# Optimization experiments

Measured on AMD Instinct MI355X. Metric: run time of the kernel, lower is better.

The kernel has to match this reference:

```python
import jax, jax.numpy as jnp
import numpy as np
from jax import lax

D = 1024      # embedding_dim
E = 8         # num_experts
F = 4096      # expert_dim
TOP_K = 2


def setup_inputs() -> dict:
    key = jax.random.key(0)
    ks = jax.random.split(key, 8)
    s = 0.02
    return {
        "x": jax.random.normal(ks[0], (4, 2048, D), dtype=jnp.float32),
        "gate_w": jax.random.normal(ks[1], (D, E), dtype=jnp.float32) * s,
        "gate_b": jnp.zeros((E,), dtype=jnp.float32),
        "w1": jax.random.normal(ks[2], (E, D, F), dtype=jnp.float32) * s,
        "b1": jnp.zeros((E, F), dtype=jnp.float32),
        "w2": jax.random.normal(ks[3], (E, F, D), dtype=jnp.float32) * s,
        "b2": jnp.zeros((E, D), dtype=jnp.float32),
    }


def reference(x, gate_w, gate_b, w1, b1, w2, b2):
    B, S, _ = x.shape
    flat = x.reshape(-1, D)                      # [T, D]
    T = flat.shape[0]

    # Router: top-k gating with softmax over the selected logits (in fp32)
    logits = flat @ gate_w + gate_b              # [T, E]
    topv, topi = lax.top_k(logits, TOP_K)        # [T, K]
    topw = jax.nn.softmax(topv.astype(jnp.float32), axis=-1).astype(x.dtype)
    routing = jnp.zeros_like(logits).at[jnp.arange(T)[:, None], topi].set(topw)  # [T, E]

    # Per-expert MLP, combined with routing weights (zeros for unselected experts
    # reproduce the masked gather/scatter of the original exactly).
    def body(acc, params):
        W1e, b1e, W2e, b2e, we = params          # we: [T]
        h = jax.nn.gelu(flat @ W1e + b1e, approximate=False)  # [T, F]
        out = h @ W2e + b2e                      # [T, D]
        return acc + out * we[:, None], None

    init = jnp.zeros_like(flat)
    final, _ = lax.scan(body, init, (w1, b1, w2, b2, routing.T))
    return final.reshape(B, S, D)
```

## Files before the change

### kernel.cpp

```cpp
#include <hip/hip_runtime.h>
#include <hip/hip_bf16.h>
#include <math.h>


#define TK 8192
#define DDIM 1024
#define FDIM 4096
#define NEXP 8
#define MAXT128 136

typedef unsigned short u16;
typedef __attribute__((ext_vector_type(8))) short bf16x8;
typedef __attribute__((ext_vector_type(4))) float f32x4;

typedef const __attribute__((address_space(1))) unsigned int* gp_u32;
typedef __attribute__((address_space(3))) unsigned int* lp_u32;

__device__ __forceinline__ u16 f2bf(float f) {
  unsigned x = __float_as_uint(f);
  x += 0x7fffu + ((x >> 16) & 1u);
  return (u16)(x >> 16);
}

__device__ __forceinline__ float fast_gelu(float v) {
  float p = v * (1.5957691216f + 0.0713548162f * v * v);
  float t = __expf(p);
  return v * t * __builtin_amdgcn_rcpf(t + 1.0f);
}

__device__ __forceinline__ bf16x8 ldfrag(const char* base, int row, int slot) {
  return *(const bf16x8*)(base + row * 128 + ((slot ^ (row & 7)) << 4));
}

__global__ void router_kernel(const float* __restrict__ x, const float* __restrict__ gw,
                              const float* __restrict__ gb,
                              int* __restrict__ top_e, float* __restrict__ top_w) {
  const int t = blockIdx.x;
  const int l = threadIdx.x;
  const float* xr = x + (size_t)t * DDIM;
  float acc[8] = {0, 0, 0, 0, 0, 0, 0, 0};
  for (int k = l; k < DDIM; k += 64) {
    float xv = xr[k];
    const float4* g4 = (const float4*)(gw + (size_t)k * 8);
    float4 ga = g4[0], gbv = g4[1];
    acc[0] = fmaf(xv, ga.x, acc[0]);  acc[1] = fmaf(xv, ga.y, acc[1]);
    acc[2] = fmaf(xv, ga.z, acc[2]);  acc[3] = fmaf(xv, ga.w, acc[3]);
    acc[4] = fmaf(xv, gbv.x, acc[4]); acc[5] = fmaf(xv, gbv.y, acc[5]);
    acc[6] = fmaf(xv, gbv.z, acc[6]); acc[7] = fmaf(xv, gbv.w, acc[7]);
  }
#pragma unroll
  for (int e = 0; e < 8; ++e)
#pragma unroll
    for (int m = 32; m; m >>= 1) acc[e] += __shfl_xor(acc[e], m, 64);
  if (l == 0) {
    float lg[8];
#pragma unroll
    for (int e = 0; e < 8; ++e) lg[e] = acc[e] + gb[e];
    int i1 = 0;
#pragma unroll
    for (int e = 1; e < 8; ++e) if (lg[e] > lg[i1]) i1 = e;
    int i2 = (i1 == 0) ? 1 : 0;
#pragma unroll
    for (int e = 0; e < 8; ++e) if (e != i1 && lg[e] > lg[i2]) i2 = e;
    float e2 = __expf(lg[i2] - lg[i1]);
    float inv = 1.0f / (1.0f + e2);
    top_e[2 * t] = i1;      top_e[2 * t + 1] = i2;
    top_w[2 * t] = inv;     top_w[2 * t + 1] = e2 * inv;
  }
}

__global__ void count_kernel(const int* __restrict__ top_e, int* __restrict__ counts) {
  __shared__ int lc[8];
  if (threadIdx.x < 8) lc[threadIdx.x] = 0;
  __syncthreads();
  int t = blockIdx.x * 256 + threadIdx.x;
  if (t < TK) {
    atomicAdd(&lc[top_e[2 * t]], 1);
    atomicAdd(&lc[top_e[2 * t + 1]], 1);
  }
  __syncthreads();
  if (threadIdx.x < 8) atomicAdd(&counts[threadIdx.x], lc[threadIdx.x]);
}

__global__ void scan_kernel(const int* __restrict__ counts, int* __restrict__ seg,
                            int* __restrict__ cur, int* __restrict__ nt128,
                            int* __restrict__ map128) {
  if (threadIdx.x == 0) {
    int s = 0, i128 = 0;
    for (int e = 0; e < 8; ++e) {
      seg[e] = s; cur[e] = s;
      int c = counts[e];
      for (int mt = 0; mt * 128 < c; ++mt) map128[i128++] = (e << 16) | mt;
      s += c;
    }
    seg[8] = s;
    *nt128 = i128;
  }
}

__global__ void scatter_kernel(const int* __restrict__ top_e, const float* __restrict__ top_w,
                               int* __restrict__ cur, int* __restrict__ tok_ids,
                               float* __restrict__ tok_wt, int* __restrict__ inv) {
  __shared__ int lcnt[8];
  __shared__ int lbase[8];
  if (threadIdx.x < 8) lcnt[threadIdx.x] = 0;
  __syncthreads();
  int t = blockIdx.x * 256 + threadIdx.x;
  int e[2]; float wv[2]; int lpos[2];
  bool valid = t < TK;
  if (valid) {
#pragma unroll
    for (int j = 0; j < 2; ++j) {
      e[j] = top_e[2 * t + j];
      wv[j] = top_w[2 * t + j];
      lpos[j] = atomicAdd(&lcnt[e[j]], 1);
    }
  }
  __syncthreads();
  if (threadIdx.x < 8) lbase[threadIdx.x] = atomicAdd(&cur[threadIdx.x], lcnt[threadIdx.x]);
  __syncthreads();
  if (valid) {
#pragma unroll
    for (int j = 0; j < 2; ++j) {
      int slot = lbase[e[j]] + lpos[j];
      tok_ids[slot] = t;
      tok_wt[slot] = wv[j];
      inv[2 * t + j] = slot;
    }
  }
}

__global__ void gather_cast_kernel(const float* __restrict__ x, const int* __restrict__ tok_ids,
                                   uint4* __restrict__ Xg) {
  int idx = blockIdx.x * 256 + threadIdx.x;
  int row = idx >> 7, c8 = (idx & 127) * 8;
  long tok = tok_ids[row];
  const float4* p = (const float4*)(x + tok * DDIM + c8);
  float4 a = p[0], b = p[1];
  uint4 o;
  o.x = (unsigned)f2bf(a.x) | ((unsigned)f2bf(a.y) << 16);
  o.y = (unsigned)f2bf(a.z) | ((unsigned)f2bf(a.w) << 16);
  o.z = (unsigned)f2bf(b.x) | ((unsigned)f2bf(b.y) << 16);
  o.w = (unsigned)f2bf(b.z) | ((unsigned)f2bf(b.w) << 16);
  Xg[idx] = o;
}

__global__ void transpose_cast_kernel(const float* __restrict__ src, u16* __restrict__ dst,
                                      int K, int N) {
  __shared__ u16 tile[64][66];
  const int t = threadIdx.x;
  const float* s = src + (size_t)blockIdx.z * K * N + (size_t)(blockIdx.x * 64) * N + blockIdx.y * 64;
  u16* d = dst + (size_t)blockIdx.z * N * K + (size_t)(blockIdx.y * 64) * K + blockIdx.x * 64;
#pragma unroll
  for (int r = 0; r < 4; ++r) {
    int idx = r * 256 + t;
    int kk = idx >> 4, nn4 = (idx & 15) * 4;
    float4 v = *(const float4*)(s + (size_t)kk * N + nn4);
    tile[kk][nn4 + 0] = f2bf(v.x);
    tile[kk][nn4 + 1] = f2bf(v.y);
    tile[kk][nn4 + 2] = f2bf(v.z);
    tile[kk][nn4 + 3] = f2bf(v.w);
  }
  __syncthreads();
#pragma unroll
  for (int r = 0; r < 2; ++r) {
    int idx = r * 256 + t;
    int nn = idx >> 3, kk8 = (idx & 7) * 8;
    uint4 o;
    o.x = (unsigned)tile[kk8 + 0][nn] | ((unsigned)tile[kk8 + 1][nn] << 16);
    o.y = (unsigned)tile[kk8 + 2][nn] | ((unsigned)tile[kk8 + 3][nn] << 16);
    o.z = (unsigned)tile[kk8 + 4][nn] | ((unsigned)tile[kk8 + 5][nn] << 16);
    o.w = (unsigned)tile[kk8 + 6][nn] | ((unsigned)tile[kk8 + 7][nn] << 16);
    *(uint4*)(d + (size_t)nn * K + kk8) = o;
  }
}

template <int PHASE, int BM, int BN, int CHA, int CHB>
__global__ __launch_bounds__(256, 4) void moe_gemm(
    const u16* __restrict__ A, const u16* __restrict__ Bt,
    const float* __restrict__ bias, u16* __restrict__ Hout,
    u16* __restrict__ Yout,
    const int* __restrict__ seg_off, const int* __restrict__ counts,
    const int* __restrict__ ntiles, const int* __restrict__ tile_map,
    int K, int N) {
  constexpr int MF = BM / 32;
  constexpr int NF = BN / 32;

  const int NTm = *ntiles;
  const int nb = N / BN;
  const int nwg = NTm * nb;
  const int bid = (int)blockIdx.x;
  if (bid >= nwg) return;
  const int q = nwg >> 3, rr = nwg & 7;
  const int xcd = bid & 7, pos = bid >> 3;
  const int work = xcd * q + (xcd < rr ? xcd : rr) + pos;
  const int mtIdx = work / nb;
  const int n0 = (work % nb) * BN;

  const int ent = tile_map[mtIdx];
  const int e = ent >> 16;
  const int mt = ent & 0xffff;
  const int cnt = counts[e];
  const int seg = seg_off[e];

  const int t = threadIdx.x;
  const int w = t >> 6;
  const int l = t & 63;
  const int lr = l & 15, lh = l >> 4;
  const int wr = w >> 1, wc = w & 1;

  __shared__ u16 As[BM * 64];
  __shared__ u16 Bs[BN * 64];

  const u16* aga[CHA];
  const u16* bga[CHB];
  const u16* Bte = Bt + (size_t)e * N * K;
#pragma unroll
  for (int j = 0; j < CHA; ++j) {
    int c = t + 256 * j;
    int row = c >> 3;
    int js = (c & 7) ^ (row & 7);
    int m = mt * BM + row;
    if (m >= cnt) m = cnt - 1;
    aga[j] = A + (size_t)(seg + m) * K + js * 8;
  }
#pragma unroll
  for (int j = 0; j < CHB; ++j) {
    int c = t + 256 * j;
    int row = c >> 3;
    int js = (c & 7) ^ (row & 7);
    bga[j] = Bte + (size_t)(n0 + row) * K + js * 8;
  }

  f32x4 acc[MF][NF];
#pragma unroll
  for (int i = 0; i < MF; ++i)
#pragma unroll
    for (int j = 0; j < NF; ++j) acc[i][j] = (f32x4){0.f, 0.f, 0.f, 0.f};

  const int NT = K / 64;
  for (int kt = 0; kt < NT; ++kt) {
#pragma unroll
    for (int j = 0; j < CHA; ++j)
      __builtin_amdgcn_global_load_lds((gp_u32)(aga[j] + (size_t)kt * 64),
                                       (lp_u32)(&As[(t + 256 * j) * 8]), 16, 0, 0);
#pragma unroll
    for (int j = 0; j < CHB; ++j)
      __builtin_amdgcn_global_load_lds((gp_u32)(bga[j] + (size_t)kt * 64),
                                       (lp_u32)(&Bs[(t + 256 * j) * 8]), 16, 0, 0);
    __syncthreads();

    const char* AsB = (const char*)As;
    const char* BsB = (const char*)Bs;
#pragma unroll
    for (int kk = 0; kk < 2; ++kk) {
      const int slot = kk * 4 + lh;
      bf16x8 a[MF], b[NF];
#pragma unroll
      for (int mi = 0; mi < MF; ++mi)
        a[mi] = ldfrag(AsB, wr * (BM / 2) + mi * 16 + lr, slot);
#pragma unroll
      for (int ni = 0; ni < NF; ++ni)
        b[ni] = ldfrag(BsB, wc * (BN / 2) + ni * 16 + lr, slot);
#pragma unroll
      for (int ni = 0; ni < NF; ++ni)
#pragma unroll
        for (int mi = 0; mi < MF; ++mi)
          acc[mi][ni] = __builtin_amdgcn_mfma_f32_16x16x32_bf16(b[ni], a[mi], acc[mi][ni], 0, 0, 0);
    }
    __syncthreads();
  }

  const float* be = bias + (size_t)e * N;
  u16* dst = (PHASE == 1) ? Hout : Yout;
#pragma unroll
  for (int mi = 0; mi < MF; ++mi) {
    int m = mt * BM + wr * (BM / 2) + mi * 16 + lr;
    if (m < cnt) {
      size_t orow = (size_t)(seg + m) * N;
#pragma unroll
      for (int ni = 0; ni < NF; ++ni) {
        int col = n0 + wc * (BN / 2) + ni * 16 + lh * 4;
        float4 bv = *(const float4*)(be + col);
        float v0 = acc[mi][ni][0] + bv.x;
        float v1 = acc[mi][ni][1] + bv.y;
        float v2 = acc[mi][ni][2] + bv.z;
        float v3 = acc[mi][ni][3] + bv.w;
        if (PHASE == 1) {
          v0 = fast_gelu(v0); v1 = fast_gelu(v1);
          v2 = fast_gelu(v2); v3 = fast_gelu(v3);
        }
        uint2 o;
        o.x = (unsigned)f2bf(v0) | ((unsigned)f2bf(v1) << 16);
        o.y = (unsigned)f2bf(v2) | ((unsigned)f2bf(v3) << 16);
        *(uint2*)(dst + orow + col) = o;
      }
    }
  }
}

__global__ void combine_kernel(const u16* __restrict__ Y, const int* __restrict__ inv,
                               const float* __restrict__ top_w, float* __restrict__ out) {
  int idx = blockIdx.x * 256 + threadIdx.x;
  int t = idx >> 7, c = (idx & 127) * 8;
  int s0 = inv[2 * t], s1 = inv[2 * t + 1];
  float w0 = top_w[2 * t], w1 = top_w[2 * t + 1];
  const uint4 y0 = *(const uint4*)(Y + (size_t)s0 * DDIM + c);
  const uint4 y1 = *(const uint4*)(Y + (size_t)s1 * DDIM + c);
  float4 o0, o1;
#define LO(u) __uint_as_float((u) << 16)
#define HI(u) __uint_as_float((u) & 0xffff0000u)
  o0.x = w0 * LO(y0.x) + w1 * LO(y1.x); o0.y = w0 * HI(y0.x) + w1 * HI(y1.x);
  o0.z = w0 * LO(y0.y) + w1 * LO(y1.y); o0.w = w0 * HI(y0.y) + w1 * HI(y1.y);
  o1.x = w0 * LO(y0.z) + w1 * LO(y1.z); o1.y = w0 * HI(y0.z) + w1 * HI(y1.z);
  o1.z = w0 * LO(y0.w) + w1 * LO(y1.w); o1.w = w0 * HI(y0.w) + w1 * HI(y1.w);
#undef LO
#undef HI
  float4* op = (float4*)(out + (size_t)t * DDIM + c);
  op[0] = o0; op[1] = o1;
}

extern "C" void kernel_launch(void* const* d_in, const int* in_sizes, int n_in,
                              void* d_out, int out_size, void* d_ws, size_t ws_size,
                              hipStream_t stream) {
  const float* x  = (const float*)d_in[0];
  const float* gw = (const float*)d_in[1];
  const float* gb = (const float*)d_in[2];
  const float* w1 = (const float*)d_in[3];
  const float* b1 = (const float*)d_in[4];
  const float* w2 = (const float*)d_in[5];
  const float* b2 = (const float*)d_in[6];
  float* out = (float*)d_out;

  char* ws = (char*)d_ws;
  int*   counts  = (int*)(ws + 0);
  int*   cursors = (int*)(ws + 64);
  int*   seg     = (int*)(ws + 128);
  int*   nt128   = (int*)(ws + 192);
  int*   map128  = (int*)(ws + 1024);
  int*   top_e   = (int*)(ws + 4096);
  float* top_w   = (float*)(ws + 4096 + 65536);
  int*   tok_ids = (int*)(ws + 4096 + 131072);
  float* tok_wt  = (float*)(ws + 4096 + 196608);
  int*   invm    = (int*)(ws + 4096 + 262144);
  u16*   Xg      = (u16*)(ws + ((size_t)1 << 20));
  u16*   Y       = (u16*)(ws + ((size_t)1 << 20));
  u16*   H       = (u16*)(ws + ((size_t)36 << 20));
  u16*   wt      = (u16*)(ws + ((size_t)164 << 20));

  hipMemsetAsync(ws, 0, 256, stream);

  router_kernel<<<TK, 64, 0, stream>>>(x, gw, gb, top_e, top_w);
  count_kernel<<<TK / 256, 256, 0, stream>>>(top_e, counts);
  scan_kernel<<<1, 64, 0, stream>>>(counts, seg, cursors, nt128, map128);
  scatter_kernel<<<TK / 256, 256, 0, stream>>>(top_e, top_w, cursors, tok_ids, tok_wt, invm);
  gather_cast_kernel<<<2 * TK * 128 / 256, 256, 0, stream>>>(x, tok_ids, (uint4*)Xg);

  transpose_cast_kernel<<<dim3(DDIM / 64, FDIM / 64, NEXP), 256, 0, stream>>>(w1, wt, DDIM, FDIM);
  moe_gemm<1, 128, 128, 4, 4><<<dim3(MAXT128 * (FDIM / 128)), 256, 0, stream>>>(
      Xg, wt, b1, H, nullptr, seg, counts, nt128, map128, DDIM, FDIM);
  transpose_cast_kernel<<<dim3(FDIM / 64, DDIM / 64, NEXP), 256, 0, stream>>>(w2, wt, FDIM, DDIM);

  moe_gemm<3, 128, 128, 4, 4><<<dim3(MAXT128 * (DDIM / 128)), 256, 0, stream>>>(
      H, wt, b2, nullptr, Y, seg, counts, nt128, map128, FDIM, DDIM);
  combine_kernel<<<TK * 128 / 256, 256, 0, stream>>>(Y, invm, top_w, out);
}
```

Baseline: 481.1 us.

## Add double-buffered LDS pipelined GEMM variant for first expert GEMM

Introduces moe_gemm_pipe, which uses two LDS buffers and prefetches the k-tile two steps ahead via global_load_lds, waiting with partial vmcnt so loads overlap MFMA compute. Only the first (up-projection + GELU) GEMM is switched to it. The intent is to hide global-memory latency behind compute. In exchange it doubles LDS use per block (64 KB), which may lower occupancy from the launch bound of 4 blocks per CU.

```diff
diff --git a/kernel.cpp b/kernel.cpp
--- a/kernel.cpp
+++ b/kernel.cpp
@@ -172,6 +172,142 @@
     o.z = (unsigned)tile[kk8 + 4][nn] | ((unsigned)tile[kk8 + 5][nn] << 16);
     o.w = (unsigned)tile[kk8 + 6][nn] | ((unsigned)tile[kk8 + 7][nn] << 16);
     *(uint4*)(d + (size_t)nn * K + kk8) = o;
+  }
+}
+
+template <int PHASE, int BM, int BN, int CHA, int CHB>
+__global__ __launch_bounds__(256, 4) void moe_gemm_pipe(
+    const u16* __restrict__ A, const u16* __restrict__ Bt,
+    const float* __restrict__ bias, u16* __restrict__ Hout,
+    u16* __restrict__ Yout,
+    const int* __restrict__ seg_off, const int* __restrict__ counts,
+    const int* __restrict__ ntiles, const int* __restrict__ tile_map,
+    int K, int N) {
+  constexpr int MF = BM / 32;
+  constexpr int NF = BN / 32;
+
+  const int NTm = *ntiles;
+  const int nb = N / BN;
+  const int nwg = NTm * nb;
+  const int bid = (int)blockIdx.x;
+  if (bid >= nwg) return;
+  const int q = nwg >> 3, rr = nwg & 7;
+  const int xcd = bid & 7, pos = bid >> 3;
+  const int work = xcd * q + (xcd < rr ? xcd : rr) + pos;
+  const int mtIdx = work / nb;
+  const int n0 = (work % nb) * BN;
+
+  const int ent = tile_map[mtIdx];
+  const int e = ent >> 16;
+  const int mt = ent & 0xffff;
+  const int cnt = counts[e];
+  const int seg = seg_off[e];
+
+  const int t = threadIdx.x;
+  const int w = t >> 6;
+  const int l = t & 63;
+  const int lr = l & 15, lh = l >> 4;
+  const int wr = w >> 1, wc = w & 1;
+
+  __shared__ u16 As[2][BM * 64];
+  __shared__ u16 Bs[2][BN * 64];
+
+  const u16* aga[CHA];
+  const u16* bga[CHB];
+  const u16* Bte = Bt + (size_t)e * N * K;
+#pragma unroll
+  for (int j = 0; j < CHA; ++j) {
+    int c = t + 256 * j;
+    int row = c >> 3;
+    int js = (c & 7) ^ (row & 7);
+    int m = mt * BM + row;
+    if (m >= cnt) m = cnt - 1;
+    aga[j] = A + (size_t)(seg + m) * K + js * 8;
+  }
+#pragma unroll
+  for (int j = 0; j < CHB; ++j) {
+    int c = t + 256 * j;
+    int row = c >> 3;
+    int js = (c & 7) ^ (row & 7);
+    bga[j] = Bte + (size_t)(n0 + row) * K + js * 8;
+  }
+
+  auto STAGE = [&](int buf, int kt) {
+#pragma unroll
+    for (int j = 0; j < CHA; ++j)
+      __builtin_amdgcn_global_load_lds((gp_u32)(aga[j] + (size_t)kt * 64),
+                                       (lp_u32)(&As[buf][(t + 256 * j) * 8]), 16, 0, 0);
+#pragma unroll
+    for (int j = 0; j < CHB; ++j)
+      __builtin_amdgcn_global_load_lds((gp_u32)(bga[j] + (size_t)kt * 64),
+                                       (lp_u32)(&Bs[buf][(t + 256 * j) * 8]), 16, 0, 0);
+  };
+
+  f32x4 acc[MF][NF];
+#pragma unroll
+  for (int i = 0; i < MF; ++i)
+#pragma unroll
+    for (int j = 0; j < NF; ++j) acc[i][j] = (f32x4){0.f, 0.f, 0.f, 0.f};
+
+  const int NT = K / 64;
+  STAGE(0, 0);
+  STAGE(1, 1);
+
+  for (int kt = 0; kt < NT; ++kt) {
+    if (kt + 1 < NT)
+      asm volatile("s_waitcnt vmcnt(8)" ::: "memory");
+    else
+      asm volatile("s_waitcnt vmcnt(0)" ::: "memory");
+    __builtin_amdgcn_s_barrier();
+
+    const char* AsB = (const char*)&As[kt & 1][0];
+    const char* BsB = (const char*)&Bs[kt & 1][0];
+#pragma unroll
+    for (int kk = 0; kk < 2; ++kk) {
+      const int slot = kk * 4 + lh;
+      bf16x8 a[MF], b[NF];
+#pragma unroll
+      for (int mi = 0; mi < MF; ++mi)
+        a[mi] = ldfrag(AsB, wr * (BM / 2) + mi * 16 + lr, slot);
+#pragma unroll
+      for (int ni = 0; ni < NF; ++ni)
+        b[ni] = ldfrag(BsB, wc * (BN / 2) + ni * 16 + lr, slot);
+#pragma unroll
+      for (int ni = 0; ni < NF; ++ni)
+#pragma unroll
+        for (int mi = 0; mi < MF; ++mi)
+          acc[mi][ni] = __builtin_amdgcn_mfma_f32_16x16x32_bf16(b[ni], a[mi], acc[mi][ni], 0, 0, 0);
+    }
+    asm volatile("s_waitcnt lgkmcnt(0)" ::: "memory");
+    __builtin_amdgcn_s_barrier();
+    if (kt + 2 < NT) STAGE(kt & 1, kt + 2);
+  }
+
+  const float* be = bias + (size_t)e * N;
+  u16* dst = (PHASE == 1) ? Hout : Yout;
+#pragma unroll
+  for (int mi = 0; mi < MF; ++mi) {
+    int m = mt * BM + wr * (BM / 2) + mi * 16 + lr;
+    if (m < cnt) {
+      size_t orow = (size_t)(seg + m) * N;
+#pragma unroll
+      for (int ni = 0; ni < NF; ++ni) {
+        int col = n0 + wc * (BN / 2) + ni * 16 + lh * 4;
+        float4 bv = *(const float4*)(be + col);
+        float v0 = acc[mi][ni][0] + bv.x;
+        float v1 = acc[mi][ni][1] + bv.y;
+        float v2 = acc[mi][ni][2] + bv.z;
+        float v3 = acc[mi][ni][3] + bv.w;
+        if (PHASE == 1) {
+          v0 = fast_gelu(v0); v1 = fast_gelu(v1);
+          v2 = fast_gelu(v2); v3 = fast_gelu(v3);
+        }
+        uint2 o;
+        o.x = (unsigned)f2bf(v0) | ((unsigned)f2bf(v1) << 16);
+        o.y = (unsigned)f2bf(v2) | ((unsigned)f2bf(v3) << 16);
+        *(uint2*)(dst + orow + col) = o;
+      }
+    }
   }
 }
 
@@ -357,7 +493,7 @@
   gather_cast_kernel<<<2 * TK * 128 / 256, 256, 0, stream>>>(x, tok_ids, (uint4*)Xg);
 
   transpose_cast_kernel<<<dim3(DDIM / 64, FDIM / 64, NEXP), 256, 0, stream>>>(w1, wt, DDIM, FDIM);
-  moe_gemm<1, 128, 128, 4, 4><<<dim3(MAXT128 * (FDIM / 128)), 256, 0, stream>>>(
+  moe_gemm_pipe<1, 128, 128, 4, 4><<<dim3(MAXT128 * (FDIM / 128)), 256, 0, stream>>>(
       Xg, wt, b1, H, nullptr, seg, counts, nt128, map128, DDIM, FDIM);
   transpose_cast_kernel<<<dim3(FDIM / 64, DDIM / 64, NEXP), 256, 0, stream>>>(w2, wt, FDIM, DDIM);
 
```

Result: slower. 531.3 us (+10.4%).
